# Kernel tuning notes

Measured on AMD Instinct MI355X. Metric: run time of the kernel, lower is better.

Reference implementation:

```python
import jax, jax.numpy as jnp
import numpy as np

EMBED = 1024
HEADS = 16
HEAD_DIM = EMBED // HEADS
N, L = 8, 1024


def setup_inputs() -> dict:
    key = jax.random.key(0)
    ks = jax.random.split(key, 12)
    s = 1.0 / np.sqrt(EMBED)
    return {
        "values": jax.random.normal(ks[0], (N, L, EMBED), jnp.float32),
        "keys": jax.random.normal(ks[1], (N, L, EMBED), jnp.float32),
        "queries": jax.random.normal(ks[2], (N, L, EMBED), jnp.float32),
        "mask": jax.random.randint(ks[3], (N, 1, L, L), 0, 2, jnp.int32),
        "Wv": jax.random.normal(ks[4], (EMBED, EMBED), jnp.float32) * s,
        "bv": jnp.zeros((EMBED,), jnp.float32),
        "Wk": jax.random.normal(ks[5], (EMBED, EMBED), jnp.float32) * s,
        "bk": jnp.zeros((EMBED,), jnp.float32),
        "Wq": jax.random.normal(ks[6], (EMBED, EMBED), jnp.float32) * s,
        "bq": jnp.zeros((EMBED,), jnp.float32),
        "Wo": jax.random.normal(ks[7], (EMBED, EMBED), jnp.float32) * s,
        "bo": jnp.zeros((EMBED,), jnp.float32),
    }


def reference(values, keys, queries, mask, Wv, bv, Wk, bk, Wq, bq, Wo, bo):
    n, q_len = queries.shape[0], queries.shape[1]
    # Linear projections (torch Linear: x @ W.T + b)
    v = values @ Wv.T + bv
    k = keys @ Wk.T + bk
    q = queries @ Wq.T + bq
    # split heads: [N, L, H, D]
    v = v.reshape(n, -1, HEADS, HEAD_DIM)
    k = k.reshape(n, -1, HEADS, HEAD_DIM)
    q = q.reshape(n, q_len, HEADS, HEAD_DIM)
    # energy: [N, H, Q, K]
    energy = jnp.einsum("nqhd,nkhd->nhqk", q, k)
    energy = jnp.where(mask == 0, jnp.float32(-1e20), energy)
    attention = jax.nn.softmax(energy / jnp.sqrt(jnp.float32(EMBED)), axis=3)
    out = jnp.einsum("nhqk,nkhd->nqhd", attention, v).reshape(n, q_len, EMBED)
    return out @ Wo.T + bo
```

## Files before the change

kernel.cpp:

```cpp
#include <hip/hip_runtime.h>
#include <hip/hip_bf16.h>


typedef __attribute__((ext_vector_type(8))) short short8;
typedef __attribute__((ext_vector_type(8))) __bf16 bf16x8;
typedef __attribute__((ext_vector_type(4))) float f32x4;
typedef __attribute__((ext_vector_type(16))) float f32x16;

static __device__ __forceinline__ unsigned short f2bf(float x) {
  union { float f; unsigned u; } v; v.f = x;
  unsigned r = v.u + 0x7FFFu + ((v.u >> 16) & 1u);
  return (unsigned short)(r >> 16);
}

static __device__ __forceinline__ f32x4 mfma16(short8 a, short8 b, f32x4 c) {
  return __builtin_amdgcn_mfma_f32_16x16x32_bf16(
      __builtin_bit_cast(bf16x8, a), __builtin_bit_cast(bf16x8, b), c, 0, 0, 0);
}
static __device__ __forceinline__ f32x16 mfma32(short8 a, short8 b, f32x16 c) {
  return __builtin_amdgcn_mfma_f32_32x32x16_bf16(
      __builtin_bit_cast(bf16x8, a), __builtin_bit_cast(bf16x8, b), c, 0, 0, 0);
}

static __device__ __forceinline__ void gll16(const unsigned short* g, unsigned short* l) {
  __builtin_amdgcn_global_load_lds(
      (const __attribute__((address_space(1))) unsigned int*)(const void*)g,
      (__attribute__((address_space(3))) unsigned int*)(void*)l, 16, 0, 0);
}

static __device__ __forceinline__ unsigned cvtpk(float lo, float hi) {
  unsigned r;
  asm("v_cvt_pk_bf16_f32 %0, %1, %2" : "=v"(r) : "v"(lo), "v"(hi));
  return r;
}

static __device__ __forceinline__ void cvt8(const float* __restrict__ in,
                                            unsigned short* __restrict__ out, int i) {
  float4 a = ((const float4*)in)[i * 2];
  float4 b = ((const float4*)in)[i * 2 + 1];
  union { short8 v; unsigned short u[8]; } pk;
  pk.u[0] = f2bf(a.x); pk.u[1] = f2bf(a.y); pk.u[2] = f2bf(a.z); pk.u[3] = f2bf(a.w);
  pk.u[4] = f2bf(b.x); pk.u[5] = f2bf(b.y); pk.u[6] = f2bf(b.z); pk.u[7] = f2bf(b.w);
  ((short8*)out)[i] = pk.v;
}

__global__ __launch_bounds__(256)
void fused_pre(const float* __restrict__ queries, const float* __restrict__ keys,
               const float* __restrict__ values,
               const float* __restrict__ Wq, const float* __restrict__ Wk,
               const float* __restrict__ Wv, const float* __restrict__ Wo,
               const int* __restrict__ mask,
               unsigned short* __restrict__ Xq, unsigned short* __restrict__ Xk,
               unsigned short* __restrict__ Xv,
               unsigned short* __restrict__ W4, unsigned long long* __restrict__ M64)
{
  const int bid = blockIdx.x, tid = threadIdx.x;
  if (bid < 4096) {
    cvt8(queries, Xq, bid * 256 + tid);
  } else if (bid < 8192) {
    cvt8(keys, Xk, (bid - 4096) * 256 + tid);
  } else if (bid < 10240) {
    const int wsel = (bid - 8192) >> 9;
    const float* src = wsel == 0 ? Wq : wsel == 1 ? Wk : wsel == 2 ? Wv : Wo;
    cvt8(src, W4 + wsel * 1048576, ((bid - 8192) & 511) * 256 + tid);
  } else if (bid < 11264) {
    const int lane = tid & 63, wid = tid >> 6;
    const int gw = (bid - 10240) * 4 + wid;
#pragma unroll 4
    for (int j = 0; j < 32; ++j) {
      const int w = gw * 32 + j;
      unsigned long long b = __ballot(mask[(size_t)w * 64 + lane] != 0);
      if (lane == 0) M64[w] = b;
    }
  } else {
    cvt8(values, Xv, (bid - 11264) * 256 + tid);
  }
}

template<int MODE>
__global__ __launch_bounds__(256)
void gemm_kernel(const unsigned short* __restrict__ A, const unsigned short* __restrict__ B,
                 const float* __restrict__ bias, void* __restrict__ outp, float oscale)
{
  __shared__ alignas(16) unsigned short As[2][8192];
  __shared__ alignas(16) unsigned short Bs[2][8192];
  const int tid = threadIdx.x, lane = tid & 63, wid = tid >> 6;
  const int l15 = lane & 15, lg = lane >> 4;
  const int j = blockIdx.x >> 3;
  int bm, bn;
  if (MODE == 3) { bn = (blockIdx.x & 7) * 8 + (j & 7); bm = j >> 3; }
  else           { bm = (blockIdx.x & 7) * 8 + (j & 7); bn = j >> 3; }
  const int wr = (wid >> 1) * 64, wc = (wid & 1) * 64;

  f32x4 acc[4][4] = {};

  const unsigned short* gA[4];
  const unsigned short* gB[4];
  unsigned short* lA[4];
  unsigned short* lB[4];
#pragma unroll
  for (int i = 0; i < 4; ++i) {
    const int so = i * 2048 + tid * 8;
    const int row = so >> 6;
    const int ch = (so >> 3) & 7;
    const int scol = (ch ^ (row & 7)) * 8;
    gA[i] = A + (size_t)(bm * 128 + row) * 1024 + scol;
    gB[i] = B + (size_t)(bn * 128 + row) * 1024 + scol;
    lA[i] = &As[0][0] + so;
    lB[i] = &Bs[0][0] + so;
  }

#pragma unroll
  for (int i = 0; i < 4; ++i) { gll16(gA[i], lA[i]); gll16(gB[i], lB[i]); }

  int cur = 0;
#pragma unroll 2
  for (int k0 = 0; k0 < 1024; k0 += 64) {
    __syncthreads();
    if (k0 + 64 < 1024) {
      const int nb = (cur ^ 1) * 8192;
#pragma unroll
      for (int i = 0; i < 4; ++i) {
        gll16(gA[i] + k0 + 64, lA[i] + nb);
        gll16(gB[i] + k0 + 64, lB[i] + nb);
      }
    }
    const unsigned short* Ab = &As[cur][0];
    const unsigned short* Bb = &Bs[cur][0];
#pragma unroll
    for (int h = 0; h < 2; ++h) {
      short8 af[4], bf[4];
#pragma unroll
      for (int f = 0; f < 4; ++f) {
        const int ra = wr + f * 16 + l15, rb = wc + f * 16 + l15;
        af[f] = *(const short8*)&Ab[ra * 64 + (((h * 4 + lg) ^ (ra & 7)) * 8)];
        bf[f] = *(const short8*)&Bb[rb * 64 + (((h * 4 + lg) ^ (rb & 7)) * 8)];
      }
#pragma unroll
      for (int r = 0; r < 4; ++r)
#pragma unroll
        for (int c = 0; c < 4; ++c)
          acc[r][c] = mfma16(af[r], bf[c], acc[r][c]);
    }
    cur ^= 1;
  }

#pragma unroll
  for (int r = 0; r < 4; ++r) {
    const int mb = bm * 128 + wr + r * 16 + lg * 4;
#pragma unroll
    for (int c = 0; c < 4; ++c) {
      const int col = bn * 128 + wc + c * 16 + l15;
      if (MODE == 0) {
        const float bv = bias[col];
        unsigned short* O = (unsigned short*)outp;
#pragma unroll
        for (int i = 0; i < 4; ++i)
          O[(size_t)(mb + i) * 1024 + col] = f2bf((acc[r][c][i] + bv) * oscale);
      } else if (MODE == 3) {
        unsigned short* O = (unsigned short*)outp;
#pragma unroll
        for (int i = 0; i < 4; ++i)
          O[(size_t)(mb + i) * 8192 + col] = f2bf(acc[r][c][i] + bias[mb + i]);
      } else {
        const float bv = bias[col];
        float* O = (float*)outp;
#pragma unroll
        for (int i = 0; i < 4; ++i)
          O[(size_t)(mb + i) * 1024 + col] = acc[r][c][i] + bv;
      }
    }
  }
}

__global__ __launch_bounds__(256)
void attn_kernel(const unsigned short* __restrict__ Q,
                 const unsigned short* __restrict__ K,
                 const unsigned short* __restrict__ VT,
                 const unsigned long long* __restrict__ M64,
                 unsigned short* __restrict__ AO)
{
  __shared__ alignas(16) unsigned short KV[2][8192];
  const int tid = threadIdx.x, lane = tid & 63, wid = tid >> 6;
  const int l31 = lane & 31, hi = lane >> 5, hi4 = hi * 4;
  const int w = (blockIdx.x & 7) * 128 + (blockIdx.x >> 3);
  const int qt = w & 7, nh = w >> 3, h = nh & 15, n = nh >> 4;
  const int qbase = qt * 128 + wid * 32;

  const unsigned short* src[4];
  unsigned short* dst0[4];
  int tstride;
  if (wid < 2) {
#pragma unroll
    for (int i = 0; i < 4; ++i) {
      const int g = wid * 4 + i, c = g >> 1, kh = g & 1;
      src[i] = K + ((size_t)(n * 1024 + kh * 32 + l31) << 10) + h * 64 + c * 16 + hi * 8;
      dst0[i] = &KV[0][g * 512];
    }
    tstride = 64 * 1024;
  } else {
#pragma unroll
    for (int i = 0; i < 4; ++i) {
      const int g = (wid - 2) * 4 + i, kt = g >> 1, dh = g & 1;
      src[i] = VT + (size_t)(h * 64 + dh * 32 + l31) * 8192 + n * 1024 + kt * 16 + hi * 8;
      dst0[i] = &KV[0][4096 + g * 512];
    }
    tstride = 64;
  }

  short8 qf[4];
#pragma unroll
  for (int c = 0; c < 4; ++c)
    qf[c] = *(const short8*)&Q[(size_t)(n * 1024 + qbase + l31) * 1024 + h * 64 + c * 16 + hi * 8];

  const unsigned long long* Mq = M64 + (size_t)(n * 1024 + qbase + l31) * 16;
  unsigned long long mw = Mq[0], mwn = 0;

  f32x16 oacc0 = {}, oacc1 = {}, lacc = {};
  short8 ones;
#pragma unroll
  for (int j = 0; j < 8; ++j) ones[j] = (short)0x3F80;

#pragma unroll
  for (int i = 0; i < 4; ++i) gll16(src[i], dst0[i]);

  int cur = 0;
#pragma unroll 2
  for (int t = 0; t < 16; ++t) {
    __syncthreads();
    if (t < 15) {
      const size_t off = (size_t)(t + 1) * tstride;
#pragma unroll
      for (int i = 0; i < 4; ++i) gll16(src[i] + off, dst0[i] + (cur ^ 1) * 8192);
      mwn = Mq[t + 1];
    }
    const unsigned short* Kb = &KV[cur][0];

    f32x16 s0 = {}, s1 = {};
    __builtin_amdgcn_s_setprio(1);
#pragma unroll
    for (int c = 0; c < 4; ++c) {
      short8 kf0 = *(const short8*)&Kb[(c * 2 + 0) * 512 + lane * 8];
      short8 kf1 = *(const short8*)&Kb[(c * 2 + 1) * 512 + lane * 8];
      s0 = mfma32(kf0, qf[c], s0);
      s1 = mfma32(kf1, qf[c], s1);
    }
    __builtin_amdgcn_s_setprio(0);

    const unsigned wlo = (unsigned)mw >> hi4;
    const unsigned whi = (unsigned)(mw >> 32) >> hi4;
#pragma unroll
    for (int kt = 0; kt < 2; ++kt) {
      const unsigned wsh = kt ? whi : wlo;
      const f32x16& sv = kt ? s1 : s0;
      float p[16];
#pragma unroll
      for (int r = 0; r < 16; ++r) {
        const float pe = exp2f(sv[r]);
        const int pos = 8 * (r >> 2) + (r & 3);
        const int msk = ((int)(wsh << (31 - pos))) >> 31;
        p[r] = __builtin_bit_cast(float, __builtin_bit_cast(int, pe) & msk);
      }
      unsigned u[4][2];
#pragma unroll
      for (int g = 0; g < 4; ++g) {
        u[g][0] = cvtpk(p[4 * g], p[4 * g + 1]);
        u[g][1] = cvtpk(p[4 * g + 2], p[4 * g + 3]);
      }
      short8 pa0, pa1;
#pragma unroll
      for (int m = 0; m < 2; ++m) {
        unsigned a0 = u[2 * m][0], b0 = u[2 * m + 1][0];
        unsigned a1 = u[2 * m][1], b1 = u[2 * m + 1][1];
        asm("v_permlane32_swap_b32 %0, %1" : "+v"(a0), "+v"(b0));
        asm("v_permlane32_swap_b32 %0, %1" : "+v"(a1), "+v"(b1));
        union { unsigned uu[4]; short8 v; } pk;
        pk.uu[0] = a0; pk.uu[1] = a1; pk.uu[2] = b0; pk.uu[3] = b1;
        if (m == 0) pa0 = pk.v; else pa1 = pk.v;
      }
      __builtin_amdgcn_s_setprio(1);
      {
        const int g0 = (kt * 2 + 0) * 2, g1 = (kt * 2 + 1) * 2;
        short8 vf00 = *(const short8*)&Kb[4096 + (g0 + 0) * 512 + lane * 8];
        short8 vf01 = *(const short8*)&Kb[4096 + (g0 + 1) * 512 + lane * 8];
        short8 vf10 = *(const short8*)&Kb[4096 + (g1 + 0) * 512 + lane * 8];
        short8 vf11 = *(const short8*)&Kb[4096 + (g1 + 1) * 512 + lane * 8];
        oacc0 = mfma32(pa0, vf00, oacc0);
        oacc1 = mfma32(pa0, vf01, oacc1);
        lacc  = mfma32(pa0, ones, lacc);
        oacc0 = mfma32(pa1, vf10, oacc0);
        oacc1 = mfma32(pa1, vf11, oacc1);
        lacc  = mfma32(pa1, ones, lacc);
      }
      __builtin_amdgcn_s_setprio(0);
    }

    mw = mwn;
    cur ^= 1;
  }

#pragma unroll
  for (int r = 0; r < 16; ++r) {
    const int qrow = 8 * (r >> 2) + (r & 3) + hi4;
    const float rl = 1.0f / lacc[r];
    const size_t row = (size_t)(n * 1024 + qbase + qrow) * 1024 + h * 64;
    AO[row + l31]      = f2bf(oacc0[r] * rl);
    AO[row + 32 + l31] = f2bf(oacc1[r] * rl);
  }
}

extern "C" void kernel_launch(void* const* d_in, const int* in_sizes, int n_in,
                              void* d_out, int out_size, void* d_ws, size_t ws_size,
                              hipStream_t stream) {
  (void)in_sizes; (void)n_in; (void)out_size; (void)ws_size;
  const float* values  = (const float*)d_in[0];
  const float* keys    = (const float*)d_in[1];
  const float* queries = (const float*)d_in[2];
  const int*   mask    = (const int*)d_in[3];
  const float* Wv = (const float*)d_in[4];
  const float* bv = (const float*)d_in[5];
  const float* Wk = (const float*)d_in[6];
  const float* bk = (const float*)d_in[7];
  const float* Wq = (const float*)d_in[8];
  const float* bq = (const float*)d_in[9];
  const float* Wo = (const float*)d_in[10];
  const float* bo = (const float*)d_in[11];

  const size_t MB = 1u << 20;
  char* ws = (char*)d_ws;
  unsigned short* R0  = (unsigned short*)(ws);
  unsigned short* R16 = (unsigned short*)(ws + 16 * MB);
  unsigned short* Qb  = (unsigned short*)(ws + 32 * MB);
  unsigned short* Kb  = (unsigned short*)(ws + 48 * MB);
  unsigned short* W4  = (unsigned short*)(ws + 64 * MB);
  unsigned long long* M64 = (unsigned long long*)(ws + 72 * MB);
  unsigned short* Xv  = (unsigned short*)d_out;

  const dim3 b256(256);
  const float SCFULL = 0.03125f * 1.44269504089f;

  fused_pre<<<dim3(15360), b256, 0, stream>>>(
      queries, keys, values, Wq, Wk, Wv, Wo, mask, R0, R16, Xv, W4, M64);
  gemm_kernel<0><<<dim3(512), b256, 0, stream>>>(R0,  W4,           bq, (void*)Qb, SCFULL);
  gemm_kernel<0><<<dim3(512), b256, 0, stream>>>(R16, W4 + 1048576, bk, (void*)Kb, 1.0f);
  gemm_kernel<3><<<dim3(512), b256, 0, stream>>>(W4 + 2 * 1048576, Xv,
                                                 bv, (void*)R16, 1.0f);
  attn_kernel<<<dim3(1024), b256, 0, stream>>>(Qb, Kb, R16, M64, R0 );
  gemm_kernel<2><<<dim3(512), b256, 0, stream>>>(R0, W4 + 3 * 1048576, bo, d_out, 1.0f);
}
```

Before: 212.9 us.

## Triple-buffer K/V tiles in attention with prefetch distance two and explicit waitcnt

Grows the attention kernel's LDS staging from two buffers to three and issues global-to-LDS loads two tiles ahead, rotating buffer pointers each iteration. The __syncthreads at loop top is replaced by a single barrier at the end of each iteration, preceded by hand-set vmcnt waits. This is meant to hide more global load latency and drop one barrier per iteration. In exchange it uses 48KB of LDS per block, which may reduce occupancy, and the hand-counted vmcnt values must stay correct as the mask load and LDS loads interleave.

```diff
diff --git a/kernel.cpp b/kernel.cpp
--- a/kernel.cpp
+++ b/kernel.cpp
@@ -180,7 +180,7 @@
                  const unsigned long long* __restrict__ M64,
                  unsigned short* __restrict__ AO)
 {
-  __shared__ alignas(16) unsigned short KV[2][8192];
+  __shared__ alignas(16) unsigned short KV[3][8192];
   const int tid = threadIdx.x, lane = tid & 63, wid = tid >> 6;
   const int l31 = lane & 31, hi = lane >> 5, hi4 = hi * 4;
   const int w = (blockIdx.x & 7) * 128 + (blockIdx.x >> 3);
@@ -188,14 +188,14 @@
   const int qbase = qt * 128 + wid * 32;
 
   const unsigned short* src[4];
-  unsigned short* dst0[4];
-  int tstride;
+  int goff[4];
+  size_t tstride;
   if (wid < 2) {
 #pragma unroll
     for (int i = 0; i < 4; ++i) {
       const int g = wid * 4 + i, c = g >> 1, kh = g & 1;
       src[i] = K + ((size_t)(n * 1024 + kh * 32 + l31) << 10) + h * 64 + c * 16 + hi * 8;
-      dst0[i] = &KV[0][g * 512];
+      goff[i] = g * 512;
     }
     tstride = 64 * 1024;
   } else {
@@ -203,7 +203,7 @@
     for (int i = 0; i < 4; ++i) {
       const int g = (wid - 2) * 4 + i, kt = g >> 1, dh = g & 1;
       src[i] = VT + (size_t)(h * 64 + dh * 32 + l31) * 8192 + n * 1024 + kt * 16 + hi * 8;
-      dst0[i] = &KV[0][4096 + g * 512];
+      goff[i] = 4096 + g * 512;
     }
     tstride = 64;
   }
@@ -212,29 +212,36 @@
 #pragma unroll
   for (int c = 0; c < 4; ++c)
     qf[c] = *(const short8*)&Q[(size_t)(n * 1024 + qbase + l31) * 1024 + h * 64 + c * 16 + hi * 8];
-
   const unsigned long long* Mq = M64 + (size_t)(n * 1024 + qbase + l31) * 16;
-  unsigned long long mw = Mq[0], mwn = 0;
+  unsigned long long mw = Mq[0];
 
   f32x16 oacc0 = {}, oacc1 = {}, lacc = {};
   short8 ones;
 #pragma unroll
   for (int j = 0; j < 8; ++j) ones[j] = (short)0x3F80;
 
-#pragma unroll
-  for (int i = 0; i < 4; ++i) gll16(src[i], dst0[i]);
-
-  int cur = 0;
-#pragma unroll 2
+  unsigned short* bufA = &KV[0][0];
+  unsigned short* bufB = &KV[1][0];
+  unsigned short* bufC = &KV[2][0];
+
+#pragma unroll
+  for (int i = 0; i < 4; ++i) gll16(src[i], bufA + goff[i]);
+#pragma unroll
+  for (int i = 0; i < 4; ++i) gll16(src[i] + tstride, bufB + goff[i]);
+  asm volatile("s_waitcnt vmcnt(4)" ::: "memory");
+  __builtin_amdgcn_sched_barrier(0);
+  __builtin_amdgcn_s_barrier();
+  __builtin_amdgcn_sched_barrier(0);
+
   for (int t = 0; t < 16; ++t) {
-    __syncthreads();
-    if (t < 15) {
-      const size_t off = (size_t)(t + 1) * tstride;
-#pragma unroll
-      for (int i = 0; i < 4; ++i) gll16(src[i] + off, dst0[i] + (cur ^ 1) * 8192);
-      mwn = Mq[t + 1];
-    }
-    const unsigned short* Kb = &KV[cur][0];
+    unsigned long long mwn = 0;
+    if (t < 15) mwn = Mq[t + 1];
+    if (t < 14) {
+      const size_t off = (size_t)(t + 2) * tstride;
+#pragma unroll
+      for (int i = 0; i < 4; ++i) gll16(src[i] + off, bufC + goff[i]);
+    }
+    const unsigned short* Kb = bufA;
 
     f32x16 s0 = {}, s1 = {};
     __builtin_amdgcn_s_setprio(1);
@@ -295,8 +302,18 @@
       __builtin_amdgcn_s_setprio(0);
     }
 
+    if (t < 15) {
+      if (t < 14) {
+        asm volatile("s_waitcnt vmcnt(5)" ::: "memory");
+      } else {
+        asm volatile("s_waitcnt vmcnt(1)" ::: "memory");
+      }
+      __builtin_amdgcn_sched_barrier(0);
+      __builtin_amdgcn_s_barrier();
+      __builtin_amdgcn_sched_barrier(0);
+    }
     mw = mwn;
-    cur ^= 1;
+    unsigned short* tmp = bufA; bufA = bufB; bufB = bufC; bufC = tmp;
   }
 
 #pragma unroll
```

Result: slower. 218.5 us (+2.7%).
